# Kernel optimization log

Hardware: AMD Instinct MI355X
Metric: run time of the kernel (lower is better)

Reference implementation:

```python
import jax, jax.numpy as jnp
import numpy as np

T, B, IN = 256, 64, 512
HIDDEN = [512, 512, 512]
DILATIONS = [1, 2, 4]


def _lstm_scan(x, W_ih, W_hh, b_ih, b_hh):
    """Run an LSTMCell over leading time axis of x: [Td, N, D] -> [Td, N, H]."""
    H = W_hh.shape[1]
    N = x.shape[1]
    h0 = jnp.zeros((N, H), x.dtype)
    c0 = jnp.zeros((N, H), x.dtype)

    def step(carry, xt):
        h, c = carry
        gates = xt @ W_ih.T + b_ih + h @ W_hh.T + b_hh  # [N, 4H], torch order i,f,g,o
        i, f, g, o = jnp.split(gates, 4, axis=-1)
        c = jax.nn.sigmoid(f) * c + jax.nn.sigmoid(i) * jnp.tanh(g)
        h = jax.nn.sigmoid(o) * jnp.tanh(c)
        return (h, c), h

    _, hs = jax.lax.scan(step, (h0, c0), x)
    return hs


def _drnn_layer(x, rate, W_ih, W_hh, b_ih, b_hh):
    """Dilated RNN layer. x: [T, B, D] with T % rate == 0.
    Torch code concats `rate` consecutive timesteps along batch -> one dilated step;
    reshape [T,B,D] -> [T//rate, rate*B, D] reproduces exactly that layout, and the
    chunk/unroll at the end is the inverse reshape."""
    Tn, Bn, D = x.shape
    Td = Tn // rate
    xd = x.reshape(Td, rate * Bn, D)
    hs = _lstm_scan(xd, W_ih, W_hh, b_ih, b_hh)  # [Td, rate*B, H]
    return hs.reshape(Tn, Bn, W_hh.shape[1])


def setup_inputs() -> dict:
    key = jax.random.key(0)
    ks = jax.random.split(key, 1 + 4 * len(HIDDEN))
    inp = {"x": jax.random.normal(ks[0], (T, B, IN), dtype=jnp.float32)}
    in_dim = IN
    ki = 1
    for li, H in enumerate(HIDDEN):
        bound = 1.0 / np.sqrt(H)
        inp[f"W_ih{li}"] = jax.random.uniform(ks[ki + 0], (4 * H, in_dim), jnp.float32, -bound, bound)
        inp[f"W_hh{li}"] = jax.random.uniform(ks[ki + 1], (4 * H, H), jnp.float32, -bound, bound)
        inp[f"b_ih{li}"] = jax.random.uniform(ks[ki + 2], (4 * H,), jnp.float32, -bound, bound)
        inp[f"b_hh{li}"] = jax.random.uniform(ks[ki + 3], (4 * H,), jnp.float32, -bound, bound)
        ki += 4
        in_dim = H
    return inp


def reference(x,
              W_ih0, W_hh0, b_ih0, b_hh0,
              W_ih1, W_hh1, b_ih1, b_hh1,
              W_ih2, W_hh2, b_ih2, b_hh2):
    params = [(W_ih0, W_hh0, b_ih0, b_hh0),
              (W_ih1, W_hh1, b_ih1, b_hh1),
              (W_ih2, W_hh2, b_ih2, b_hh2)]
    h = x
    for (Wih, Whh, bih, bhh), rate in zip(params, DILATIONS):
        h = _drnn_layer(h, rate, Wih, Whh, bih, bhh)
    return h  # [T, B, HIDDEN[-1]]
```

## Files before the change

kernel.cpp:

```cpp
#include <hip/hip_runtime.h>

typedef __attribute__((ext_vector_type(8))) short bf16x8;
typedef __attribute__((ext_vector_type(4))) float f32x4;

__device__ __forceinline__ unsigned short f2bf(float x) {
    unsigned u = __float_as_uint(x);
    u += 0x7FFFu + ((u >> 16) & 1u);
    return (unsigned short)(u >> 16);
}
__device__ __forceinline__ float sigm(float x) { return 1.0f / (1.0f + __expf(-x)); }
__device__ __forceinline__ float ftanh(float x) {
    float e = __expf(2.f * x);
    return 1.f - 2.f / (e + 1.f);
}

__device__ __forceinline__ void gld16(const unsigned short* g, unsigned short* l) {
    __builtin_amdgcn_global_load_lds((const __attribute__((address_space(1))) void*)g,
                                     (__attribute__((address_space(3))) void*)l, 16, 0, 0);
}

__device__ __forceinline__ void st_plain32(unsigned* p, unsigned v) {
    asm volatile("global_store_dword %0, %1, off" :: "v"(p), "v"(v) : "memory");
}
__device__ __forceinline__ void st_wt32(unsigned* p, unsigned v) {
    asm volatile("global_store_dword %0, %1, off sc0 sc1" :: "v"(p), "v"(v) : "memory");
}
__device__ __forceinline__ unsigned ld_mall(const unsigned* p) {
    unsigned v;
    asm volatile("global_load_dword %0, %1, off sc0 sc1\n\ts_waitcnt vmcnt(0)"
                 : "=v"(v) : "v"(p) : "memory");
    return v;
}
__device__ __forceinline__ void st_wt16(unsigned short* p, unsigned v) {
    asm volatile("global_store_short %0, %1, off sc0 sc1" :: "v"(p), "v"(v) : "memory");
}

__device__ __forceinline__ float dppx1(float x) {
    return __int_as_float(__builtin_amdgcn_mov_dpp(__float_as_int(x), 0xB1, 0xF, 0xF, true));
}
__device__ __forceinline__ float dppx2(float x) {
    return __int_as_float(__builtin_amdgcn_mov_dpp(__float_as_int(x), 0x4E, 0xF, 0xF, true));
}

__global__ __launch_bounds__(256) void k_conv_x(const float* __restrict__ x,
                                                unsigned short* __restrict__ Xp) {
    int i = blockIdx.x * 256 + threadIdx.x;
    int rb = i >> 10, kc = (i >> 6) & 15, ln = i & 63;
    int row = (rb << 4) + (ln & 15);
    int k   = (kc << 5) + ((ln >> 4) << 3);
    const float* s = x + (size_t)row * 512 + k;
    float4 v0 = *(const float4*)s, v1 = *(const float4*)(s + 4);
    unsigned short o[8] = {f2bf(v0.x), f2bf(v0.y), f2bf(v0.z), f2bf(v0.w),
                           f2bf(v1.x), f2bf(v1.y), f2bf(v1.z), f2bf(v1.w)};
    *(bf16x8*)(Xp + (size_t)i * 8) = *(bf16x8*)o;
}

__global__ __launch_bounds__(256) void k_conv_w(const float* __restrict__ Wih,
                                                const float* __restrict__ Whh,
                                                unsigned short* __restrict__ Wp) {
    int i = blockIdx.x * 256 + threadIdx.x;
    int wrb = i >> 11, kc = (i >> 6) & 31, ln = i & 63;
    int j = (wrb << 4) + (ln & 15);
    int k = (kc << 5) + ((ln >> 4) << 3);
    int srow = (j & 3) * 512 + (j >> 2);
    const float* s = (k < 512) ? (Wih + (size_t)srow * 512 + k)
                               : (Whh + (size_t)srow * 512 + (k - 512));
    float4 v0 = *(const float4*)s, v1 = *(const float4*)(s + 4);
    unsigned short o[8] = {f2bf(v0.x), f2bf(v0.y), f2bf(v0.z), f2bf(v0.w),
                           f2bf(v1.x), f2bf(v1.y), f2bf(v1.z), f2bf(v1.w)};
    *(bf16x8*)(Wp + (size_t)i * 8) = *(bf16x8*)o;
}

struct DP {
    const unsigned short* Xp;
    unsigned short *Hp0, *Hp1, *Hp2;
    unsigned short *Xq1, *Xq2;
    const unsigned short *Wp0, *Wp1, *Wp2;
    const float *bi0, *bh0, *bi1, *bh1, *bi2, *bh2;
    float* Out;
    unsigned int* flags;
};

__device__ __forceinline__ void quadT(f32x4 a, int sq, float& G0, float& G1, float& G2, float& G3) {
    float a0 = a[0], a1 = a[1], a2 = a[2], a3 = a[3];
    float p1 = (sq & 1) ? a0 : a1; float g1_ = dppx1(p1);
    float p2 = (sq & 1) ? a2 : a3; float g2_ = dppx1(p2);
    float m0 = (sq & 1) ? g1_ : a0, m1 = (sq & 1) ? a1 : g1_;
    float m2 = (sq & 1) ? g2_ : a2, m3 = (sq & 1) ? a3 : g2_;
    float q1 = (sq & 2) ? m0 : m2; float h1_ = dppx2(q1);
    float q2 = (sq & 2) ? m1 : m3; float h2_ = dppx2(q2);
    G0 = (sq & 2) ? h1_ : m0; G1 = (sq & 2) ? h2_ : m1;
    G2 = (sq & 2) ? m2 : h1_; G3 = (sq & 2) ? m3 : h2_;
}

#define PIN8(A,B,C,D,E,F,G,H) \
    asm volatile("" : "+v"(A),"+v"(B),"+v"(C),"+v"(D),"+v"(E),"+v"(F),"+v"(G),"+v"(H))
#define SBAR()  __builtin_amdgcn_sched_barrier(0)
#define MEMBAR() asm volatile("" ::: "memory")
#define RAWBAR() do { MEMBAR(); SBAR(); __builtin_amdgcn_s_barrier(); SBAR(); MEMBAR(); } while (0)
#define VMC(n) asm volatile("s_waitcnt vmcnt(" #n ")" ::: "memory")

__global__ __launch_bounds__(256, 1) void k_drnn(DP p) {
    const int tid = threadIdx.x, lane = tid & 63, wv = tid >> 6;
    const int l15 = lane & 15, lhi = lane >> 4, sq = l15 & 3;

    const int b = blockIdx.x;
    const int cid = b & 7, w = b >> 3;
    int l, c, T, P, N;
    if (cid < 2)      { l = 0; c = cid;     T = 256; P = 1; N = 64;  }
    else if (cid < 4) { l = 1; c = cid - 2; T = 128; P = 2; N = 128; }
    else              { l = 2; c = cid - 4; T = 64;  P = 2; N = 256; }

    const unsigned short* Xs = (l == 0) ? p.Xp  : (l == 1 ? p.Xq1 : p.Xq2);
    unsigned short*       Hd = (l == 0) ? p.Hp0 : (l == 1 ? p.Hp1 : p.Hp2);
    unsigned short*       Xw = (l == 0) ? p.Xq1 : (l == 1 ? p.Xq2 : nullptr);
    const unsigned short* Ws = (l == 0) ? p.Wp0 : (l == 1 ? p.Wp1 : p.Wp2);
    const float* bi = (l == 0) ? p.bi0 : (l == 1 ? p.bi1 : p.bi2);
    const float* bh = (l == 0) ? p.bh0 : (l == 1 ? p.bh1 : p.bh2);
    const int R0 = c * (P * 32);
    const int alias = (p.Xq1 == p.Hp0);

    __shared__ unsigned short At[65536];
    __shared__ unsigned pollbuf[128];

    const unsigned short* wbase = Ws + ((size_t)(((w << 2) + wv) * 32) << 9) + lane * 8;
#define DECLW(n) bf16x8 w##n = *(const bf16x8*)(wbase + (n << 9));
    DECLW(0) DECLW(1) DECLW(2) DECLW(3) DECLW(4) DECLW(5) DECLW(6) DECLW(7)
    DECLW(8) DECLW(9) DECLW(10) DECLW(11) DECLW(12) DECLW(13) DECLW(14) DECLW(15)
    DECLW(16) DECLW(17) DECLW(18) DECLW(19) DECLW(20) DECLW(21) DECLW(22) DECLW(23)
    DECLW(24) DECLW(25) DECLW(26) DECLW(27) DECLW(28) DECLW(29) DECLW(30) DECLW(31)

    const int hcol = (w << 4) + (wv << 2) + (l15 >> 2);
    const float bs0 = bi[hcol]        + bh[hcol];
    const float bs1 = bi[512 + hcol]  + bh[512 + hcol];
    const float bs2 = bi[1024 + hcol] + bh[1024 + hcol];
    const float bs3 = bi[1536 + hcol] + bh[1536 + hcol];

    const int kch = hcol >> 5;
    const int lane16 = (((hcol & 31) >> 3) << 4) + ((lhi << 2) + sq);
    const int st_lt = lane16 * 8 + (hcol & 7);

    float cst0 = 0.f, cst1 = 0.f, cst2 = 0.f, cst3 = 0.f;
    unsigned int* iflagL = p.flags;
    unsigned int* mflagL = p.flags + 8192;
    int fastok = 1;

#define KPX(na, nb, E0, E1, O0, O1, A0, A1) { \
    bf16x8 xa = *(const bf16x8*)((A0) + ((na) << 9)); \
    bf16x8 xb = *(const bf16x8*)((A1) + ((na) << 9)); \
    bf16x8 ya = *(const bf16x8*)((A0) + ((nb) << 9)); \
    bf16x8 yb = *(const bf16x8*)((A1) + ((nb) << 9)); \
    E0 = __builtin_amdgcn_mfma_f32_16x16x32_bf16(xa, w##na, E0, 0, 0, 0); \
    E1 = __builtin_amdgcn_mfma_f32_16x16x32_bf16(xb, w##na, E1, 0, 0, 0); \
    O0 = __builtin_amdgcn_mfma_f32_16x16x32_bf16(ya, w##nb, O0, 0, 0, 0); \
    O1 = __builtin_amdgcn_mfma_f32_16x16x32_bf16(yb, w##nb, O1, 0, 0, 0); }

#define XH(E0, E1, O0, O1, A0, A1) \
    KPX(0,1,E0,E1,O0,O1,A0,A1) KPX(2,3,E0,E1,O0,O1,A0,A1) \
    KPX(4,5,E0,E1,O0,O1,A0,A1) KPX(6,7,E0,E1,O0,O1,A0,A1) \
    KPX(8,9,E0,E1,O0,O1,A0,A1) KPX(10,11,E0,E1,O0,O1,A0,A1) \
    KPX(12,13,E0,E1,O0,O1,A0,A1) KPX(14,15,E0,E1,O0,O1,A0,A1)
#define HH(E0, E1, O0, O1, A0, A1) \
    KPX(16,17,E0,E1,O0,O1,A0,A1) KPX(18,19,E0,E1,O0,O1,A0,A1) \
    KPX(20,21,E0,E1,O0,O1,A0,A1) KPX(22,23,E0,E1,O0,O1,A0,A1) \
    KPX(24,25,E0,E1,O0,O1,A0,A1) KPX(26,27,E0,E1,O0,O1,A0,A1) \
    KPX(28,29,E0,E1,O0,O1,A0,A1) KPX(30,31,E0,E1,O0,O1,A0,A1)

#define PWC(RV, CSTV, HV) { \
    float G0, G1, G2, G3; quadT(RV, sq, G0, G1, G2, G3); \
    float cn = sigm(G1 + bs1) * CSTV + sigm(G0 + bs0) * ftanh(G2 + bs2); \
    HV = sigm(G3 + bs3) * ftanh(cn); CSTV = cn; }

#define STAGE_X(TT) { \
    const int RxN = ((TT) * N + R0) >> 4; \
    for (int i = 0; i < P * 8; ++i) { \
        int q = wv * (P * 8) + i, rb = q >> 4, kc = q & 15; \
        gld16(Xs + ((size_t)((RxN + rb) * 16 + kc) << 9) + lane * 8, \
              &At[(rb * 32 + kc) << 9]); } }
#define STAGE_H(TT) { \
    const int RhN = ((TT) * N + R0) >> 4; \
    for (int i = 0; i < P * 8; ++i) { \
        int q = wv * (P * 8) + i, rb = q >> 4, kc = q & 15; \
        gld16(Hd + ((size_t)((RhN + rb) * 16 + kc) << 9) + lane * 8, \
              &At[(rb * 32 + 16 + kc) << 9]); } }

#define MPOLL(TT) { \
    if (l == 1 && wv == 1) { \
        const unsigned* mp = mflagL + ((((lane >> 5) << 5) + (lane & 31)) << 5); \
        unsigned nd = (unsigned)(2 * (TT) + c + 2); if (nd > 256u) nd = 256u; \
        int n = 0; \
        while (!__all(ld_mall(mp) >= nd)) { if (++n > (1 << 22)) break; } \
    } \
    if (l == 2 && wv == 1) { \
        const unsigned* mp = mflagL + ((((2 + (c & 1)) << 5) + (lane & 31)) << 5); \
        unsigned nd = (unsigned)(2 * (TT) + (c >> 1) + 2); if (nd > 128u) nd = 128u; \
        int n = 0; \
        while (!__all(ld_mall(mp) >= nd)) { if (++n > (1 << 22)) break; } \
    } }

    f32x4 e0 = {0,0,0,0}, e1 = {0,0,0,0}, o0 = {0,0,0,0}, o1 = {0,0,0,0};
    f32x4 e2 = {0,0,0,0}, e3 = {0,0,0,0}, o2 = {0,0,0,0}, o3 = {0,0,0,0};
    const unsigned short* A00 = At + lane * 8;
    const unsigned short* A01 = A00 + (32 << 9);
    const unsigned short* A10 = A00 + (64 << 9);
    const unsigned short* A11 = A00 + (96 << 9);

    MPOLL(0);
    RAWBAR();
    STAGE_X(0);
    VMC(0);
    RAWBAR();
    { XH(e0, e1, o0, o1, A00, A01) }
    if (P == 2) { XH(e2, e3, o2, o3, A10, A11) }

    for (int t = 0; t < T; ++t) {
        PIN8(w0,w1,w2,w3,w4,w5,w6,w7);
        PIN8(w8,w9,w10,w11,w12,w13,w14,w15);
        PIN8(w16,w17,w18,w19,w20,w21,w22,w23);
        PIN8(w24,w25,w26,w27,w28,w29,w30,w31);

        const int RxB = (t * N + R0) >> 4;

        if (t > 0) {
            if (wv == 0) {
                const unsigned need = (unsigned)t;
                const unsigned* mp = mflagL + (((cid << 5) + (lane & 31)) << 5);
                if (t == T - 1 || !fastok) {
                    int n = 0;
                    while (!__all(ld_mall(mp) >= need)) { if (++n > (1 << 22)) break; }
                } else {
                    const unsigned short* gip =
                        (const unsigned short*)(iflagL + (((cid << 5) + (lane & 31)) << 5));
                    volatile unsigned* pb = pollbuf;
                    int n = 0;
                    for (;;) {
                        if (lane < 32) gld16(gip, (unsigned short*)pollbuf);
                        VMC(0);
                        SBAR();
                        unsigned v = pb[(lane & 31) * 4];
                        if (__all((v - need) <= 1u)) break;
                        if (++n > 1024) {
                            fastok = 0;
                            int m = 0;
                            while (!__all(ld_mall(mp) >= need)) { if (++m > (1 << 22)) break; }
                            break;
                        }
                    }
                }
            }
            RAWBAR();
            STAGE_H(t - 1);
            VMC(0);
            RAWBAR();
            { HH(e0, e1, o0, o1, A00, A01) }
            if (P == 2) { HH(e2, e3, o2, o3, A10, A11) }
        }

        float hv0, hv1, hv2 = 0.f, hv3 = 0.f;
        { f32x4 r0 = e0 + o0, r1 = e1 + o1;
          PWC(r0, cst0, hv0) PWC(r1, cst1, hv1) }
        if (P == 2) {
          f32x4 r2 = e2 + o2, r3 = e3 + o3;
          PWC(r2, cst2, hv2) PWC(r3, cst3, hv3) }

        const unsigned short hb0 = f2bf(hv0), hb1 = f2bf(hv1);
        const unsigned short hb2 = f2bf(hv2), hb3 = f2bf(hv3);
        const size_t i0 = ((size_t)((RxB + 0) * 16 + kch) << 9) + st_lt;
        const size_t i1 = ((size_t)((RxB + 1) * 16 + kch) << 9) + st_lt;
        const size_t i2 = ((size_t)((RxB + 2) * 16 + kch) << 9) + st_lt;
        const size_t i3 = ((size_t)((RxB + 3) * 16 + kch) << 9) + st_lt;

        if (!alias || l == 2) {
            Hd[i0] = hb0; Hd[i1] = hb1;
            if (P == 2) { Hd[i2] = hb2; Hd[i3] = hb3; }
        }
        if (alias && l < 2) {
            st_wt16(Xw + i0, hb0); st_wt16(Xw + i1, hb1);
            if (P == 2) { st_wt16(Xw + i2, hb2); st_wt16(Xw + i3, hb3); }
        }
        if (l == 2) {
            p.Out[((size_t)(((RxB + 0) << 4) + (lhi << 2) + sq)) * 512 + hcol] = hv0;
            p.Out[((size_t)(((RxB + 1) << 4) + (lhi << 2) + sq)) * 512 + hcol] = hv1;
            p.Out[((size_t)(((RxB + 2) << 4) + (lhi << 2) + sq)) * 512 + hcol] = hv2;
            p.Out[((size_t)(((RxB + 3) << 4) + (lhi << 2) + sq)) * 512 + hcol] = hv3;
        }
        MEMBAR(); SBAR();

        if (t + 1 < T) {
            if (l == 0) {
                if (t == 0) RAWBAR();
                STAGE_X(t + 1);
                if (!alias) { st_wt16(Xw + i0, hb0); st_wt16(Xw + i1, hb1); }
                MEMBAR(); SBAR();
                if (!alias) VMC(10);
                else        VMC(8);
                RAWBAR();
                if (tid == 192) {
                    st_plain32(iflagL + (((cid << 5) + w) << 5), (unsigned)(t + 1));
                    st_wt32(mflagL + (((cid << 5) + w) << 5), (unsigned)(t + 1));
                }
                MEMBAR(); SBAR();
                if (!alias) { if (wv == 3) VMC(4); else VMC(2); }
                else        { if (wv == 3) VMC(2); else VMC(0); }
            } else {
                MPOLL(t + 1);
                VMC(0);
                RAWBAR();
                STAGE_X(t + 1);
                if (l == 1 && !alias) {
                    st_wt16(Xw + i0, hb0); st_wt16(Xw + i1, hb1);
                    st_wt16(Xw + i2, hb2); st_wt16(Xw + i3, hb3);
                }
                MEMBAR(); SBAR();
                if (tid == 192) {
                    st_plain32(iflagL + (((cid << 5) + w) << 5), (unsigned)(t + 1));
                    st_wt32(mflagL + (((cid << 5) + w) << 5), (unsigned)(t + 1));
                }
                MEMBAR(); SBAR();
                if (l == 1 && !alias) { if (wv == 3) VMC(6); else VMC(4); }
                else                  { if (wv == 3) VMC(2); else VMC(0); }
            }
            RAWBAR();
            e0 = (f32x4){0,0,0,0}; e1 = (f32x4){0,0,0,0};
            o0 = (f32x4){0,0,0,0}; o1 = (f32x4){0,0,0,0};
            { XH(e0, e1, o0, o1, A00, A01) }
            if (P == 2) {
                e2 = (f32x4){0,0,0,0}; e3 = (f32x4){0,0,0,0};
                o2 = (f32x4){0,0,0,0}; o3 = (f32x4){0,0,0,0};
                XH(e2, e3, o2, o3, A10, A11)
            }
        } else {
            if (!alias && l == 0) { st_wt16(Xw + i0, hb0); st_wt16(Xw + i1, hb1); }
            if (!alias && l == 1) { st_wt16(Xw + i0, hb0); st_wt16(Xw + i1, hb1);
                                    st_wt16(Xw + i2, hb2); st_wt16(Xw + i3, hb3); }
            MEMBAR(); SBAR();
            VMC(0);
            RAWBAR();
        }
    }

    VMC(0);
    __builtin_amdgcn_s_barrier();
    if (tid == 192) {
        st_plain32(iflagL + (((cid << 5) + w) << 5), (unsigned)T);
        st_wt32(mflagL + (((cid << 5) + w) << 5), (unsigned)T);
    }
}

extern "C" void kernel_launch(void* const* d_in, const int* in_sizes, int n_in,
                              void* d_out, int out_size, void* d_ws, size_t ws_size,
                              hipStream_t stream)
{
    const float* x = (const float*)d_in[0];
    const float* Wih[3] = {(const float*)d_in[1], (const float*)d_in[5], (const float*)d_in[9]};
    const float* Whh[3] = {(const float*)d_in[2], (const float*)d_in[6], (const float*)d_in[10]};
    const float* bih[3] = {(const float*)d_in[3], (const float*)d_in[7], (const float*)d_in[11]};
    const float* bhh[3] = {(const float*)d_in[4], (const float*)d_in[8], (const float*)d_in[12]};

    char* wp = (char*)d_ws;
    const size_t SZ_A = (size_t)16384 * 512;
    unsigned int* flags = (unsigned int*)wp; wp += 65536;
    unsigned short* Xp  = (unsigned short*)wp; wp += SZ_A * 2;
    unsigned short* Hp0 = (unsigned short*)wp; wp += SZ_A * 2;
    unsigned short* Hp1 = (unsigned short*)wp; wp += SZ_A * 2;
    unsigned short* Hp2 = (unsigned short*)wp; wp += SZ_A * 2;
    unsigned short* Wp[3];
    for (int l = 0; l < 3; ++l) { Wp[l] = (unsigned short*)wp; wp += (size_t)2048 * 1024 * 2; }
    unsigned short* Xq1 = (unsigned short*)wp; wp += SZ_A * 2;
    unsigned short* Xq2 = (unsigned short*)wp; wp += SZ_A * 2;
    const size_t need = (size_t)(wp - (char*)d_ws);
    if (ws_size < need) { Xq1 = Hp0; Xq2 = Hp1; }

    hipMemsetAsync(flags, 0, 65536, stream);
    k_conv_x<<<dim3(4096), dim3(256), 0, stream>>>(x, Xp);
    for (int l = 0; l < 3; ++l)
        k_conv_w<<<dim3(1024), dim3(256), 0, stream>>>(Wih[l], Whh[l], Wp[l]);

    DP dp;
    dp.Xp = Xp; dp.Hp0 = Hp0; dp.Hp1 = Hp1; dp.Hp2 = Hp2;
    dp.Xq1 = Xq1; dp.Xq2 = Xq2;
    dp.Wp0 = Wp[0]; dp.Wp1 = Wp[1]; dp.Wp2 = Wp[2];
    dp.bi0 = bih[0]; dp.bh0 = bhh[0];
    dp.bi1 = bih[1]; dp.bh1 = bhh[1];
    dp.bi2 = bih[2]; dp.bh2 = bhh[2];
    dp.Out = (float*)d_out; dp.flags = flags;

    k_drnn<<<dim3(256), dim3(256), 0, stream>>>(dp);
}
```

Baseline: 897.6 us.

## Publish per-wave progress flags so consumers wait on each wave individually

Each wave now writes its own progress flag (lane 0 of every wave) instead of one thread per block writing after a block barrier. The VMC wait before flag publication no longer needs to cover all waves via a barrier. Pollers read four flags per block (two lanes times two adjacent slots) so they can see every producing wave. This removes the block-wide barrier from the signal path so fast waves publish sooner, at the cost of more polling loads per check.

```diff
diff --git a/kernel.cpp b/kernel.cpp
--- a/kernel.cpp
+++ b/kernel.cpp
@@ -121,7 +121,7 @@
     const int alias = (p.Xq1 == p.Hp0);
 
     __shared__ unsigned short At[65536];
-    __shared__ unsigned pollbuf[128];
+    __shared__ unsigned pollbuf[256];
 
     const unsigned short* wbase = Ws + ((size_t)(((w << 2) + wv) * 32) << 9) + lane * 8;
 #define DECLW(n) bf16x8 w##n = *(const bf16x8*)(wbase + (n << 9));
@@ -143,6 +143,8 @@
     float cst0 = 0.f, cst1 = 0.f, cst2 = 0.f, cst3 = 0.f;
     unsigned int* iflagL = p.flags;
     unsigned int* mflagL = p.flags + 8192;
+    unsigned int* myIf = iflagL + (((cid << 5) + w) << 5) + wv;
+    unsigned int* myMf = mflagL + (((cid << 5) + w) << 5) + wv;
     int fastok = 1;
 
 #define KPX(na, nb, E0, E1, O0, O1, A0, A1) { \
@@ -186,16 +188,26 @@
 
 #define MPOLL(TT) { \
     if (l == 1 && wv == 1) { \
-        const unsigned* mp = mflagL + ((((lane >> 5) << 5) + (lane & 31)) << 5); \
         unsigned nd = (unsigned)(2 * (TT) + c + 2); if (nd > 256u) nd = 256u; \
+        const unsigned* q0 = mflagL + ((0 + (lane >> 1)) << 5) + ((lane & 1) << 1); \
+        const unsigned* q1 = mflagL + (((32 + (lane >> 1))) << 5) + ((lane & 1) << 1); \
         int n = 0; \
-        while (!__all(ld_mall(mp) >= nd)) { if (++n > (1 << 22)) break; } \
+        for (;;) { \
+            unsigned a = ld_mall(q0), bb = ld_mall(q0 + 1); \
+            unsigned cc = ld_mall(q1), dd = ld_mall(q1 + 1); \
+            if (__all(a >= nd && bb >= nd && cc >= nd && dd >= nd)) break; \
+            if (++n > (1 << 22)) break; \
+        } \
     } \
     if (l == 2 && wv == 1) { \
-        const unsigned* mp = mflagL + ((((2 + (c & 1)) << 5) + (lane & 31)) << 5); \
         unsigned nd = (unsigned)(2 * (TT) + (c >> 1) + 2); if (nd > 128u) nd = 128u; \
+        const unsigned* q0 = mflagL + ((((2 + (c & 1)) << 5) + (lane >> 1)) << 5) + ((lane & 1) << 1); \
         int n = 0; \
-        while (!__all(ld_mall(mp) >= nd)) { if (++n > (1 << 22)) break; } \
+        for (;;) { \
+            unsigned a = ld_mall(q0), bb = ld_mall(q0 + 1); \
+            if (__all(a >= nd && bb >= nd)) break; \
+            if (++n > (1 << 22)) break; \
+        } \
     } }
 
     f32x4 e0 = {0,0,0,0}, e1 = {0,0,0,0}, o0 = {0,0,0,0}, o1 = {0,0,0,0};
@@ -224,25 +236,35 @@
         if (t > 0) {
             if (wv == 0) {
                 const unsigned need = (unsigned)t;
-                const unsigned* mp = mflagL + (((cid << 5) + (lane & 31)) << 5);
+                const unsigned* mp = mflagL + (((cid << 5) + (lane >> 1)) << 5) + ((lane & 1) << 1);
                 if (t == T - 1 || !fastok) {
                     int n = 0;
-                    while (!__all(ld_mall(mp) >= need)) { if (++n > (1 << 22)) break; }
+                    for (;;) {
+                        unsigned a = ld_mall(mp), bb = ld_mall(mp + 1);
+                        if (__all(a >= need && bb >= need)) break;
+                        if (++n > (1 << 22)) break;
+                    }
                 } else {
                     const unsigned short* gip =
                         (const unsigned short*)(iflagL + (((cid << 5) + (lane & 31)) << 5));
                     volatile unsigned* pb = pollbuf;
                     int n = 0;
                     for (;;) {
-                        if (lane < 32) gld16(gip, (unsigned short*)pollbuf);
+                        gld16(gip, (unsigned short*)pollbuf);
                         VMC(0);
                         SBAR();
-                        unsigned v = pb[(lane & 31) * 4];
-                        if (__all((v - need) <= 1u)) break;
+                        const int bse = (lane & 31) * 4;
+                        unsigned v0 = pb[bse + 0] - need, v1 = pb[bse + 1] - need;
+                        unsigned v2 = pb[bse + 2] - need, v3 = pb[bse + 3] - need;
+                        if (__all(v0 <= 1u && v1 <= 1u && v2 <= 1u && v3 <= 1u)) break;
                         if (++n > 1024) {
                             fastok = 0;
                             int m = 0;
-                            while (!__all(ld_mall(mp) >= need)) { if (++m > (1 << 22)) break; }
+                            for (;;) {
+                                unsigned a = ld_mall(mp), bb = ld_mall(mp + 1);
+                                if (__all(a >= need && bb >= need)) break;
+                                if (++m > (1 << 22)) break;
+                            }
                             break;
                         }
                     }
@@ -292,16 +314,13 @@
                 STAGE_X(t + 1);
                 if (!alias) { st_wt16(Xw + i0, hb0); st_wt16(Xw + i1, hb1); }
                 MEMBAR(); SBAR();
-                if (!alias) VMC(10);
-                else        VMC(8);
-                RAWBAR();
-                if (tid == 192) {
-                    st_plain32(iflagL + (((cid << 5) + w) << 5), (unsigned)(t + 1));
-                    st_wt32(mflagL + (((cid << 5) + w) << 5), (unsigned)(t + 1));
+                if (!alias) VMC(10); else VMC(8);
+                if (lane == 0) {
+                    st_plain32(myIf, (unsigned)(t + 1));
+                    st_wt32(myMf, (unsigned)(t + 1));
                 }
                 MEMBAR(); SBAR();
-                if (!alias) { if (wv == 3) VMC(4); else VMC(2); }
-                else        { if (wv == 3) VMC(2); else VMC(0); }
+                if (!alias) VMC(4); else VMC(2);
             } else {
                 MPOLL(t + 1);
                 VMC(0);
@@ -312,13 +331,12 @@
                     st_wt16(Xw + i2, hb2); st_wt16(Xw + i3, hb3);
                 }
                 MEMBAR(); SBAR();
-                if (tid == 192) {
-                    st_plain32(iflagL + (((cid << 5) + w) << 5), (unsigned)(t + 1));
-                    st_wt32(mflagL + (((cid << 5) + w) << 5), (unsigned)(t + 1));
+                if (lane == 0) {
+                    st_plain32(myIf, (unsigned)(t + 1));
+                    st_wt32(myMf, (unsigned)(t + 1));
                 }
                 MEMBAR(); SBAR();
-                if (l == 1 && !alias) { if (wv == 3) VMC(6); else VMC(4); }
-                else                  { if (wv == 3) VMC(2); else VMC(0); }
+                if (l == 1 && !alias) VMC(6); else VMC(2);
             }
             RAWBAR();
             e0 = (f32x4){0,0,0,0}; e1 = (f32x4){0,0,0,0};
@@ -341,9 +359,9 @@
 
     VMC(0);
     __builtin_amdgcn_s_barrier();
-    if (tid == 192) {
-        st_plain32(iflagL + (((cid << 5) + w) << 5), (unsigned)T);
-        st_wt32(mflagL + (((cid << 5) + w) << 5), (unsigned)T);
+    if (lane == 0) {
+        st_plain32(myIf, (unsigned)T);
+        st_wt32(myMf, (unsigned)T);
     }
 }
 
```

After: 1.075 ms. +19.8%, slower.
